# Optimization experiments

Hardware: AMD Instinct MI355X
Metric: run time of the kernel (lower is better)

## Reference

```python
import itertools
import jax, jax.numpy as jnp
import numpy as np

RES = 14
B = 64
DIM = 384
NH = 8
KD = 32
DV = 128  # attn_ratio * key_dim
SCALE = KD ** -0.5


def _bias_idxs(res):
    points = list(itertools.product(range(res), range(res)))
    offs, idxs = {}, []
    for p1 in points:
        for p2 in points:
            o = (abs(p1[0] - p2[0]), abs(p1[1] - p2[1]))
            if o not in offs:
                offs[o] = len(offs)
            idxs.append(offs[o])
    n = res * res
    return np.asarray(idxs, dtype=np.int32).reshape(n, n), len(offs)


def setup_inputs() -> dict:
    key = jax.random.key(0)
    ks = jax.random.split(key, 16)
    idxs, n_off = _bias_idxs(RES)  # n_off == 196 for res=14
    f = lambda k, shape, s=0.05: jax.random.normal(k, shape, dtype=jnp.float32) * s
    return {
        "x": jax.random.normal(ks[0], (B, DIM, RES, RES), dtype=jnp.float32),
        "qw": f(ks[1], (NH * KD, DIM)), "qb": f(ks[2], (NH * KD,)),
        "kw": f(ks[3], (NH * KD, DIM)), "kb": f(ks[4], (NH * KD,)),
        "vw": f(ks[5], (NH * DV, DIM)), "vb": f(ks[6], (NH * DV,)),
        "vlw": f(ks[7], (NH * DV, 1, 3, 3)), "vlb": f(ks[8], (NH * DV,)),
        "th1_w": f(ks[9], (NH, NH), 0.3), "th1_b": f(ks[10], (NH,)),
        "th2_w": f(ks[11], (NH, NH), 0.3), "th2_b": f(ks[12], (NH,)),
        "projw": f(ks[13], (DIM, NH * DV)), "projb": f(ks[14], (DIM,)),
        "bias_seg": f(ks[15], (NH, n_off), 0.5),
        "bias_idxs": jnp.asarray(idxs),
    }


def reference(x, qw, qb, kw, kb, vw, vb, vlw, vlb,
              th1_w, th1_b, th2_w, th2_b, projw, projb,
              bias_seg, bias_idxs):
    Bb, C, H, W = x.shape
    N = H * W
    xf = x.reshape(Bb, C, N)
    # 1x1 conv (+ folded BN) projections
    q = (jnp.einsum('oc,bcn->bon', qw, xf) + qb[:, None]).reshape(Bb, NH, KD, N).transpose(0, 1, 3, 2)  # [B,h,N,kd]
    k = (jnp.einsum('oc,bcn->bon', kw, xf) + kb[:, None]).reshape(Bb, NH, KD, N)                        # [B,h,kd,N]
    v4 = (jnp.einsum('oc,bcn->bon', vw, xf) + vb[:, None]).reshape(Bb, NH * DV, H, W)
    # depthwise 3x3 local branch (+ folded BN)
    v_local = jax.lax.conv_general_dilated(
        v4, vlw, window_strides=(1, 1), padding=[(1, 1), (1, 1)],
        dimension_numbers=('NCHW', 'OIHW', 'NCHW'), feature_group_count=NH * DV,
    ) + vlb[None, :, None, None]
    v = v4.reshape(Bb, NH, DV, N).transpose(0, 1, 3, 2)  # [B,h,N,dv]
    # attention scores + relative bias (bicubic interp 196->196 is identity)
    attn = jnp.einsum('bhnk,bhkm->bhnm', q, k) * SCALE
    bias = bias_seg[:, bias_idxs]  # [h,N,N]
    attn = attn + bias[None]
    # talking heads (1x1 conv over head dim) -> softmax -> talking heads
    attn = jnp.einsum('hg,bgnm->bhnm', th1_w, attn) + th1_b[None, :, None, None]
    attn = jax.nn.softmax(attn, axis=-1)
    attn = jnp.einsum('hg,bgnm->bhnm', th2_w, attn) + th2_b[None, :, None, None]
    o = jnp.einsum('bhnm,bhmd->bhnd', attn, v)           # [B,h,N,dv]
    o = o.transpose(0, 1, 3, 2).reshape(Bb, NH * DV, H, W) + v_local
    # proj: ReLU -> 1x1 conv (+ folded BN)
    o = jax.nn.relu(o)
    out = jnp.einsum('oc,bchw->bohw', projw, o) + projb[None, :, None, None]
    return out
```

## Files before the change

kernel.cpp:

```cpp
#include <hip/hip_runtime.h>
#include <hip/hip_bf16.h>


#define RES   14
#define NSP   196
#define NHD   8
#define KDIM  32
#define DVV   128
#define DIM   384
#define NQK   256
#define SCALE 0.17677669529663687f
#define SROW  224
#define NSTRIP 13

typedef __attribute__((ext_vector_type(8))) short bf16x8;
typedef __attribute__((ext_vector_type(4))) float f32x4;
typedef unsigned short u16;
typedef unsigned int u32;

__device__ __forceinline__ u16 f2b(float f) {
    union { __hip_bfloat16 b; u16 u; } c; c.b = __float2bfloat16(f); return c.u;
}
__device__ __forceinline__ float b2f(u16 u) {
    union { __hip_bfloat16 b; u16 u; } c; c.u = u; return __bfloat162float(c.b);
}

__device__ __forceinline__ void gld16(const void* g, void* l) {
    __builtin_amdgcn_global_load_lds(
        (__attribute__((address_space(1))) void*)(unsigned long long)(const char*)g,
        (__attribute__((address_space(3))) void*)l, 16, 0, 0);
}

__device__ __forceinline__ void gemm128_bk64(const char* Aseg, long rbA,
                                             const char* Bseg, long rbB, int kIters,
                                             u16* A_lds, u16* B_lds, f32x4 acc[4][4])
{
    const int tid  = threadIdx.x;
    const int wid  = tid >> 6;
    const int lane = tid & 63;
    const int lrow = lane >> 2;
    const int lcb  = (lane & 3) << 4;
    const int r0   = wid * 32;
    const int wm   = (wid & 1) * 64, wn = (wid >> 1) * 64;
    const int l15  = lane & 15, lq8 = (lane >> 4) * 8;

    #pragma unroll
    for (int i = 0; i < 4; ++i)
        #pragma unroll
        for (int j = 0; j < 4; ++j) acc[i][j] = (f32x4){0.f, 0.f, 0.f, 0.f};

    const char* ap0 = Aseg + (long)(r0 + lrow) * rbA + lcb;
    const char* ap1 = ap0 + 16 * rbA;
    const char* bp0 = Bseg + (long)(r0 + lrow) * rbB + lcb;
    const char* bp1 = bp0 + 16 * rbB;
    u16* la0 = A_lds + r0 * 32;
    u16* la1 = la0 + 512;
    u16* lb0 = B_lds + r0 * 32;
    u16* lb1 = lb0 + 512;

    for (int kk = 0; kk < kIters; ++kk) {
        gld16(ap0, la0);        gld16(ap1, la1);
        gld16(bp0, lb0);        gld16(bp1, lb1);
        gld16(ap0 + 64, la0 + 4096); gld16(ap1 + 64, la1 + 4096);
        gld16(bp0 + 64, lb0 + 4096); gld16(bp1 + 64, lb1 + 4096);
        ap0 += 128; ap1 += 128; bp0 += 128; bp1 += 128;
        __syncthreads();
        #pragma unroll
        for (int s = 0; s < 2; ++s) {
            bf16x8 af[4], bfr[4];
            #pragma unroll
            for (int i = 0; i < 4; ++i)
                af[i] = *(const bf16x8*)&A_lds[s * 4096 + (wm + i * 16 + l15) * 32 + lq8];
            #pragma unroll
            for (int j = 0; j < 4; ++j)
                bfr[j] = *(const bf16x8*)&B_lds[s * 4096 + (wn + j * 16 + l15) * 32 + lq8];
            #pragma unroll
            for (int i = 0; i < 4; ++i)
                #pragma unroll
                for (int j = 0; j < 4; ++j)
                    acc[i][j] = __builtin_amdgcn_mfma_f32_16x16x32_bf16(
                        af[i], bfr[j], acc[i][j], 0, 0, 0);
        }
        __syncthreads();
    }
}

__global__ __launch_bounds__(256) void k_prep(
    const float* __restrict__ qw, const float* __restrict__ kw,
    const float* __restrict__ vw, const float* __restrict__ pw,
    const float* __restrict__ th1w, const float* __restrict__ th1b,
    const float* __restrict__ bias_seg, const float* __restrict__ vlw,
    const float* __restrict__ x,
    u16* __restrict__ wqkv, u16* __restrict__ pwb, float* __restrict__ biasmix,
    u16* __restrict__ wpack, u16* __restrict__ xb)
{
    __shared__ float t[32][33];
    const int bid = blockIdx.x;
    if (bid < 3883) {
        int i = bid * 256 + threadIdx.x;
        if (i < 98304)       wqkv[i] = f2b(qw[i]);
        else if (i < 196608) wqkv[i] = f2b(kw[i - 98304]);
        else if (i < 589824) wqkv[i] = f2b(vw[i - 196608]);
        else if (i < 983040) pwb[i - 589824] = f2b(pw[i - 589824]);
        else if (i < 984608) {
            int i2 = i - 983040;
            int hh = i2 / NSP, off = i2 - hh * NSP;
            float a = th1b[hh];
            #pragma unroll
            for (int g = 0; g < 8; ++g) a += th1w[hh * 8 + g] * bias_seg[g * NSP + off];
            biasmix[i2] = a;
        } else if (i < 993824) {
            int i2 = i - 984608;
            int g = i2 / 72, r = i2 - g * 72;
            int tap = r >> 3, tt = r & 7;
            wpack[i2] = f2b(vlw[(g * 8 + tt) * 9 + tap]);
        }
    } else {
        const int L = bid - 3883;
        const int b = L / 84, r = L - b * 84;
        const int c0 = (r / 7) * 32, n0 = (r % 7) * 32;
        const int tx = threadIdx.x & 31, ty = threadIdx.x >> 5;
        #pragma unroll
        for (int l = 0; l < 4; ++l) {
            int c = c0 + ty + 8 * l, n = n0 + tx;
            t[ty + 8 * l][tx] = (n < NSP) ? x[((long)b * DIM + c) * NSP + n] : 0.f;
        }
        __syncthreads();
        #pragma unroll
        for (int l = 0; l < 4; ++l) {
            int n = n0 + ty + 8 * l, c = c0 + tx;
            if (n < NSP) xb[((long)b * NSP + n) * DIM + c] = f2b(t[tx][ty + 8 * l]);
        }
    }
}

__global__ __launch_bounds__(256) void k_qkv(
    const u16* __restrict__ xb, const u16* __restrict__ wqkv,
    const float* __restrict__ qb, const float* __restrict__ kb,
    const float* __restrict__ vb,
    u16* __restrict__ qt, u16* __restrict__ kb16, u16* __restrict__ vt)
{
    __shared__ u16 A_lds[8192], B_lds[8192];
    const int m0 = blockIdx.x * 128, oc0 = blockIdx.y * 128;
    f32x4 acc[4][4];
    gemm128_bk64((const char*)xb + (long)m0 * 768, 768,
                 (const char*)wqkv + (long)oc0 * 768, 768, 6, A_lds, B_lds, acc);

    const int tid = threadIdx.x, wid = tid >> 6, lane = tid & 63;
    const int wm = (wid & 1) * 64, wn = (wid >> 1) * 64;
    const int col = lane & 15, quad = lane >> 4;
    #pragma unroll
    for (int i = 0; i < 4; ++i) {
        #pragma unroll
        for (int j = 0; j < 4; ++j) {
            #pragma unroll
            for (int r = 0; r < 4; ++r) {
                int m  = m0 + wm + i * 16 + quad * 4 + r;
                int oc = oc0 + wn + j * 16 + col;
                int b = m / NSP, n = m - b * NSP;
                float v = acc[i][j][r];
                if (oc < 256) {
                    qt[(long)m * NQK + oc] = f2b(v + qb[oc]);
                } else if (oc < 512) {
                    int o = oc - 256;
                    kb16[(long)m * NQK + o] = f2b(v + kb[o]);
                } else {
                    int o = oc - 512, h = o >> 7, d = o & 127;
                    vt[(((long)b * NHD + h) * NSP + n) * DVV + d] = f2b(v + vb[o]);
                }
            }
        }
    }
}

__global__ __launch_bounds__(256) void k_vtT(
    const u16* __restrict__ vt, u16* __restrict__ vtT)
{
    __shared__ u16 t[32][33];
    const int bh = blockIdx.z, d0 = blockIdx.y * 32, n0 = blockIdx.x * 32;
    const int tx = threadIdx.x & 31, ty = threadIdx.x >> 5;
    #pragma unroll
    for (int l = 0; l < 4; ++l) {
        int n = n0 + ty + 8 * l, d = d0 + tx;
        t[ty + 8 * l][tx] = (n < NSP) ? vt[((long)bh * NSP + n) * DVV + d] : (u16)0;
    }
    __syncthreads();
    #pragma unroll
    for (int l = 0; l < 4; ++l) {
        int d = d0 + ty + 8 * l, m = n0 + tx;
        vtT[((long)bh * DVV + d) * 224 + m] = t[tx][ty + 8 * l];
    }
}

__global__ __launch_bounds__(256) void k_dwconv(
    const u16* __restrict__ vt, const u16* __restrict__ wpack,
    const float* __restrict__ vlb, u16* __restrict__ vlt)
{
    const int tid = threadIdx.x;
    const int dg = tid & 15;
    const int nl = tid >> 4;
    const int bh = blockIdx.y;
    const int n  = blockIdx.x * 16 + nl;
    if (n >= NSP) return;
    const int d0 = dg * 8;
    const int h  = bh & 7;
    const int y = n / RES, xx = n - y * RES;
    const long plane = (long)bh * NSP * DVV;
    float acc[8];
    #pragma unroll
    for (int t = 0; t < 8; ++t) acc[t] = vlb[h * DVV + d0 + t];
    const u16* wb = wpack + (h * 16 + dg) * 72;
    #pragma unroll
    for (int dy = -1; dy <= 1; ++dy) {
        int yy = y + dy;
        if (yy < 0 || yy >= RES) continue;
        #pragma unroll
        for (int dx = -1; dx <= 1; ++dx) {
            int xn = xx + dx;
            if (xn < 0 || xn >= RES) continue;
            int tap = (dy + 1) * 3 + dx + 1;
            bf16x8 v  = *(const bf16x8*)&vt[plane + (yy * RES + xn) * DVV + d0];
            bf16x8 wv = *(const bf16x8*)&wb[tap * 8];
            #pragma unroll
            for (int t = 0; t < 8; ++t)
                acc[t] += b2f((u16)wv[t]) * b2f((u16)v[t]);
        }
    }
    bf16x8 r;
    #pragma unroll
    for (int t = 0; t < 8; ++t) r[t] = (short)f2b(acc[t]);
    *(bf16x8*)&vlt[plane + (long)n * DVV + d0] = r;
}

__global__ __launch_bounds__(512, 2) void k_attn2(
    const u16* __restrict__ qt, const u16* __restrict__ kb16,
    const u16* __restrict__ vtT, const u16* __restrict__ vlt,
    const float* __restrict__ th1w, const float* __restrict__ th2w,
    const float* __restrict__ th2b, const float* __restrict__ biasmix,
    u16* __restrict__ ot)
{
    __shared__ u16 S[128 * SROW];
    __shared__ u16 bmS[8 * NSP];
    const int tid = threadIdx.x;
    const int L  = blockIdx.x;
    const int wq = L >> 3;
    const int b  = (L & 7) + ((wq / NSTRIP) << 3);
    const int n0 = (wq % NSTRIP) * 16;
    const int wid = tid >> 6, lane = tid & 63;
    const int l15 = lane & 15, lq8 = (lane >> 4) * 8;
    const int quad = lane >> 4, col = lane & 15;

    for (int i = tid; i < 8 * NSP; i += 512) bmS[i] = f2b(biasmix[i]);
    __syncthreads();

    {
        const long qrow = ((long)(b * NSP) + n0 + l15) * NQK;
        bf16x8 af[8];
        #pragma unroll
        for (int g = 0; g < 8; ++g)
            af[g] = *(const bf16x8*)&qt[qrow + g * 32 + lq8];
        #pragma unroll
        for (int jj = 0; jj < 2; ++jj) {
            const int j = wid + jj * 8;
            if (j >= 13) break;
            const long krow = ((long)(b * NSP) + j * 16 + l15) * NQK;
            f32x4 t[8];
            #pragma unroll
            for (int g = 0; g < 8; ++g) {
                bf16x8 bv = *(const bf16x8*)&kb16[krow + g * 32 + lq8];
                t[g] = __builtin_amdgcn_mfma_f32_16x16x32_bf16(
                    af[g], bv, (f32x4){0.f, 0.f, 0.f, 0.f}, 0, 0, 0);
            }
            const int m = j * 16 + col;
            const int ym = m / RES, xm = m - ym * RES;
            int offr[4];
            #pragma unroll
            for (int r = 0; r < 4; ++r) {
                int gn = n0 + quad * 4 + r;
                int yn = gn / RES, xn = gn - yn * RES;
                int off = abs(yn - ym) * RES + abs(xn - xm);
                offr[r] = (off > 195) ? 195 : off;
            }
            #pragma unroll
            for (int h = 0; h < 8; ++h) {
                float o[4];
                #pragma unroll
                for (int r = 0; r < 4; ++r) o[r] = b2f(bmS[h * NSP + offr[r]]);
                #pragma unroll
                for (int g = 0; g < 8; ++g) {
                    const float w = th1w[h * 8 + g] * SCALE;
                    #pragma unroll
                    for (int r = 0; r < 4; ++r) o[r] += w * t[g][r];
                }
                #pragma unroll
                for (int r = 0; r < 4; ++r)
                    S[(h * 16 + quad * 4 + r) * SROW + m] = f2b(o[r]);
            }
        }
    }
    __syncthreads();

    {
        const int c = lane & 15, rg = lane >> 4;
        #pragma unroll
        for (int it = 0; it < 4; ++it) {
            u16* row = &S[(wid * 16 + it * 4 + rg) * SROW];
            float v[13];
            #pragma unroll
            for (int k = 0; k < 12; ++k) v[k] = b2f(row[c + 16 * k]);
            v[12] = (c < 4) ? b2f(row[192 + c]) : -1e30f;
            float mx = v[0];
            #pragma unroll
            for (int k = 1; k < 13; ++k) mx = fmaxf(mx, v[k]);
            #pragma unroll
            for (int o = 1; o < 16; o <<= 1) mx = fmaxf(mx, __shfl_xor(mx, o));
            float sum = 0.f;
            #pragma unroll
            for (int k = 0; k < 13; ++k) { v[k] = __expf(v[k] - mx); sum += v[k]; }
            if (c >= 4) sum -= v[12];
            #pragma unroll
            for (int o = 1; o < 16; o <<= 1) sum += __shfl_xor(sum, o);
            float inv = 1.0f / sum;
            #pragma unroll
            for (int k = 0; k < 12; ++k) row[c + 16 * k] = f2b(v[k] * inv);
            if (c < 4) row[192 + c] = f2b(v[12] * inv);
        }
    }
    __syncthreads();

    {
        for (int p = tid; p < 16 * 112; p += 512) {
            const int nl = p / 112, kp = p - nl * 112;
            const int m0 = kp * 2;
            if (m0 >= NSP) {
                #pragma unroll
                for (int h = 0; h < 8; ++h)
                    *(u32*)&S[(h * 16 + nl) * SROW + m0] = 0u;
                continue;
            }
            float s0[8], s1[8];
            #pragma unroll
            for (int g = 0; g < 8; ++g) {
                u32 v = *(const u32*)&S[(g * 16 + nl) * SROW + m0];
                s0[g] = b2f((u16)(v & 0xffff));
                s1[g] = b2f((u16)(v >> 16));
            }
            #pragma unroll
            for (int h = 0; h < 8; ++h) {
                float o0 = th2b[h], o1 = th2b[h];
                #pragma unroll
                for (int g = 0; g < 8; ++g) {
                    const float w = th2w[h * 8 + g];
                    o0 += w * s0[g];
                    o1 += w * s1[g];
                }
                *(u32*)&S[(h * 16 + nl) * SROW + m0] =
                    (u32)f2b(o0) | ((u32)f2b(o1) << 16);
            }
        }
    }
    __syncthreads();

    {
        const int h = wid;
        const long vrow = (long)(b * NHD + h) * DVV;
        f32x4 acc[8];
        #pragma unroll
        for (int df = 0; df < 8; ++df) acc[df] = (f32x4){0.f, 0.f, 0.f, 0.f};
        for (int kc = 0; kc < 7; ++kc) {
            bf16x8 a0 = *(const bf16x8*)&S[(h * 16 + l15) * SROW + kc * 32 + lq8];
            #pragma unroll
            for (int df = 0; df < 8; ++df) {
                bf16x8 bv = *(const bf16x8*)&vtT[(vrow + df * 16 + l15) * 224 + kc * 32 + lq8];
                acc[df] = __builtin_amdgcn_mfma_f32_16x16x32_bf16(a0, bv, acc[df], 0, 0, 0);
            }
        }
        const long lbase = (long)(b * NHD + h) * NSP;
        #pragma unroll
        for (int df = 0; df < 8; ++df) {
            #pragma unroll
            for (int r = 0; r < 4; ++r) {
                int n = n0 + quad * 4 + r;
                int d = df * 16 + col;
                if (n < NSP) {
                    float v = acc[df][r] + b2f(vlt[(lbase + n) * DVV + d]);
                    v = fmaxf(v, 0.f);
                    ot[((long)(b * NSP + n)) * 1024 + h * DVV + d] = f2b(v);
                }
            }
        }
    }
}

__global__ __launch_bounds__(256) void k_proj(
    const u16* __restrict__ pwb, const u16* __restrict__ ot,
    const float* __restrict__ projb, float* __restrict__ outp)
{
    __shared__ u16 A_lds[8192];
    __shared__ u16 B_lds[4096];
    const int tid = threadIdx.x, wid = tid >> 6, lane = tid & 63;
    const int lrow = lane >> 2, lcb = (lane & 3) << 4;
    const int m0 = blockIdx.x * 64, oc0 = blockIdx.y * 128;
    const int wm = (wid & 1) * 64, wn = (wid >> 1) * 32;
    const int l15 = lane & 15, lq8 = (lane >> 4) * 8;

    const char* gp[6];
    u16* lp[6];
    #pragma unroll
    for (int t = 0; t < 6; ++t) {
        int s = wid * 6 + t;
        int sub = s / 12, s12 = s - sub * 12;
        if (s12 < 8) {
            gp[t] = (const char*)pwb + (long)(oc0 + s12 * 16 + lrow) * 2048 + lcb + sub * 64;
            lp[t] = A_lds + sub * 4096 + s12 * 512;
        } else {
            gp[t] = (const char*)ot + (long)(m0 + (s12 - 8) * 16 + lrow) * 2048 + lcb + sub * 64;
            lp[t] = B_lds + sub * 2048 + (s12 - 8) * 512;
        }
    }

    f32x4 acc[4][2];
    #pragma unroll
    for (int i = 0; i < 4; ++i)
        #pragma unroll
        for (int j = 0; j < 2; ++j) acc[i][j] = (f32x4){0.f, 0.f, 0.f, 0.f};

    for (int kk = 0; kk < 16; ++kk) {
        #pragma unroll
        for (int t = 0; t < 6; ++t) { gld16(gp[t], lp[t]); gp[t] += 128; }
        __syncthreads();
        #pragma unroll
        for (int s = 0; s < 2; ++s) {
            bf16x8 af[4], bfr[2];
            #pragma unroll
            for (int i = 0; i < 4; ++i)
                af[i] = *(const bf16x8*)&A_lds[s * 4096 + (wm + i * 16 + l15) * 32 + lq8];
            #pragma unroll
            for (int j = 0; j < 2; ++j)
                bfr[j] = *(const bf16x8*)&B_lds[s * 2048 + (wn + j * 16 + l15) * 32 + lq8];
            #pragma unroll
            for (int i = 0; i < 4; ++i)
                #pragma unroll
                for (int j = 0; j < 2; ++j)
                    acc[i][j] = __builtin_amdgcn_mfma_f32_16x16x32_bf16(
                        af[i], bfr[j], acc[i][j], 0, 0, 0);
        }
        __syncthreads();
    }

    const int col = lane & 15, quad = lane >> 4;
    #pragma unroll
    for (int i = 0; i < 4; ++i) {
        #pragma unroll
        for (int j = 0; j < 2; ++j) {
            #pragma unroll
            for (int r = 0; r < 4; ++r) {
                int oc = oc0 + wm + i * 16 + quad * 4 + r;
                int mg = m0 + wn + j * 16 + col;
                int b = mg / NSP, n = mg - b * NSP;
                outp[((long)b * DIM + oc) * NSP + n] = acc[i][j][r] + projb[oc];
            }
        }
    }
}

extern "C" void kernel_launch(void* const* d_in, const int* in_sizes, int n_in,
                              void* d_out, int out_size, void* d_ws, size_t ws_size,
                              hipStream_t stream) {
    const float* x        = (const float*)d_in[0];
    const float* qw       = (const float*)d_in[1];
    const float* qb       = (const float*)d_in[2];
    const float* kw       = (const float*)d_in[3];
    const float* kb       = (const float*)d_in[4];
    const float* vw       = (const float*)d_in[5];
    const float* vb       = (const float*)d_in[6];
    const float* vlw      = (const float*)d_in[7];
    const float* vlb      = (const float*)d_in[8];
    const float* th1w     = (const float*)d_in[9];
    const float* th1b     = (const float*)d_in[10];
    const float* th2w     = (const float*)d_in[11];
    const float* th2b     = (const float*)d_in[12];
    const float* projw    = (const float*)d_in[13];
    const float* projb    = (const float*)d_in[14];
    const float* bias_seg = (const float*)d_in[15];
    float* outp = (float*)d_out;

    char* w = (char*)d_ws;
    u16* xb      = (u16*)(w);
    u16* wqkv    = (u16*)(w + 9633792);
    u16* pwb     = (u16*)(w + 10813440);
    u16* wpack   = (u16*)(w + 11599872);
    float* bmix  = (float*)(w + 11618304);
    u16* qt      = (u16*)(w + 11624704);
    u16* kb16    = (u16*)(w + 18080000);
    u16* vt      = (u16*)(w + 24535296);
    u16* vtT     = (u16*)(w + 50225408);
    u16* ot      = (u16*)(w + 79585536);
    u16* vlt     = (u16*)(w + 105275648);

    k_prep<<<dim3(9259), 256, 0, stream>>>(qw, kw, vw, projw, th1w, th1b,
                                           bias_seg, vlw, x, wqkv, pwb, bmix,
                                           wpack, xb);
    k_qkv<<<dim3(98, 12), 256, 0, stream>>>(xb, wqkv, qb, kb, vb, qt, kb16, vt);
    k_vtT<<<dim3(7, 4, 512), 256, 0, stream>>>(vt, vtT);
    k_dwconv<<<dim3(13, 512), 256, 0, stream>>>(vt, wpack, vlb, vlt);
    k_attn2<<<dim3(NSTRIP * 64), 512, 0, stream>>>(qt, kb16, vtT, vlt, th1w, th2w,
                                                   th2b, bmix, ot);
    k_proj<<<dim3(196, 3), 256, 0, stream>>>(pwb, ot, projb, outp);
}
```

Baseline: 295.0 us.

## Merge V transpose and depthwise conv kernels, prefetch operands in attention, vectorize prep

Vectorizes the weight-conversion part of k_prep to float4 loads with 4-wide bf16 stores, which cuts its block count. Merges the V transpose and depthwise-conv kernels into one launch, and has the conv write its output transposed with row stride 208. Attention now issues the K loads for the second tile early and double-buffers the V operand loads across k-chunks. The epilogue reads the local branch as 4-wide vectors. The transposed conv store is a strided scalar write, which may be less coalesced than before.

```diff
diff --git a/kernel.cpp b/kernel.cpp
--- a/kernel.cpp
+++ b/kernel.cpp
@@ -11,10 +11,12 @@
 #define NQK   256
 #define SCALE 0.17677669529663687f
 #define SROW  224
+#define VROW  208
 #define NSTRIP 13
 
 typedef __attribute__((ext_vector_type(8))) short bf16x8;
 typedef __attribute__((ext_vector_type(4))) float f32x4;
+typedef __attribute__((ext_vector_type(4))) unsigned short u16x4;
 typedef unsigned short u16;
 typedef unsigned int u32;
 
@@ -96,27 +98,34 @@
 {
     __shared__ float t[32][33];
     const int bid = blockIdx.x;
-    if (bid < 3883) {
-        int i = bid * 256 + threadIdx.x;
-        if (i < 98304)       wqkv[i] = f2b(qw[i]);
-        else if (i < 196608) wqkv[i] = f2b(kw[i - 98304]);
-        else if (i < 589824) wqkv[i] = f2b(vw[i - 196608]);
-        else if (i < 983040) pwb[i - 589824] = f2b(pw[i - 589824]);
-        else if (i < 984608) {
-            int i2 = i - 983040;
+    if (bid < 960) {
+        const int i = (bid * 256 + threadIdx.x) * 4;
+        const float* src; u16* dst;
+        if (i < 98304)       { src = qw + i;            dst = wqkv + i; }
+        else if (i < 196608) { src = kw + (i - 98304);  dst = wqkv + i; }
+        else if (i < 589824) { src = vw + (i - 196608); dst = wqkv + i; }
+        else                 { src = pw + (i - 589824); dst = pwb + (i - 589824); }
+        float4 v = *(const float4*)src;
+        u16x4 o;
+        o[0] = f2b(v.x); o[1] = f2b(v.y); o[2] = f2b(v.z); o[3] = f2b(v.w);
+        *(u16x4*)dst = o;
+    } else if (bid == 960) {
+        for (int i2 = threadIdx.x; i2 < 8 * NSP; i2 += 256) {
             int hh = i2 / NSP, off = i2 - hh * NSP;
             float a = th1b[hh];
             #pragma unroll
             for (int g = 0; g < 8; ++g) a += th1w[hh * 8 + g] * bias_seg[g * NSP + off];
             biasmix[i2] = a;
-        } else if (i < 993824) {
-            int i2 = i - 984608;
+        }
+    } else if (bid < 997) {
+        int i2 = (bid - 961) * 256 + threadIdx.x;
+        if (i2 < 9216) {
             int g = i2 / 72, r = i2 - g * 72;
             int tap = r >> 3, tt = r & 7;
             wpack[i2] = f2b(vlw[(g * 8 + tt) * 9 + tap]);
         }
     } else {
-        const int L = bid - 3883;
+        const int L = bid - 997;
         const int b = L / 84, r = L - b * 84;
         const int c0 = (r / 7) * 32, n0 = (r % 7) * 32;
         const int tx = threadIdx.x & 31, ty = threadIdx.x >> 5;
@@ -173,68 +182,72 @@
     }
 }
 
-__global__ __launch_bounds__(256) void k_vtT(
-    const u16* __restrict__ vt, u16* __restrict__ vtT)
+__global__ __launch_bounds__(256) void k_vtdw(
+    const u16* __restrict__ vt, const u16* __restrict__ wpack,
+    const float* __restrict__ vlb,
+    u16* __restrict__ vtT, u16* __restrict__ vltT)
 {
     __shared__ u16 t[32][33];
-    const int bh = blockIdx.z, d0 = blockIdx.y * 32, n0 = blockIdx.x * 32;
-    const int tx = threadIdx.x & 31, ty = threadIdx.x >> 5;
-    #pragma unroll
-    for (int l = 0; l < 4; ++l) {
-        int n = n0 + ty + 8 * l, d = d0 + tx;
-        t[ty + 8 * l][tx] = (n < NSP) ? vt[((long)bh * NSP + n) * DVV + d] : (u16)0;
-    }
-    __syncthreads();
-    #pragma unroll
-    for (int l = 0; l < 4; ++l) {
-        int d = d0 + ty + 8 * l, m = n0 + tx;
-        vtT[((long)bh * DVV + d) * 224 + m] = t[tx][ty + 8 * l];
-    }
-}
-
-__global__ __launch_bounds__(256) void k_dwconv(
-    const u16* __restrict__ vt, const u16* __restrict__ wpack,
-    const float* __restrict__ vlb, u16* __restrict__ vlt)
-{
-    const int tid = threadIdx.x;
-    const int dg = tid & 15;
-    const int nl = tid >> 4;
-    const int bh = blockIdx.y;
-    const int n  = blockIdx.x * 16 + nl;
-    if (n >= NSP) return;
-    const int d0 = dg * 8;
-    const int h  = bh & 7;
-    const int y = n / RES, xx = n - y * RES;
-    const long plane = (long)bh * NSP * DVV;
-    float acc[8];
-    #pragma unroll
-    for (int t = 0; t < 8; ++t) acc[t] = vlb[h * DVV + d0 + t];
-    const u16* wb = wpack + (h * 16 + dg) * 72;
-    #pragma unroll
-    for (int dy = -1; dy <= 1; ++dy) {
-        int yy = y + dy;
-        if (yy < 0 || yy >= RES) continue;
-        #pragma unroll
-        for (int dx = -1; dx <= 1; ++dx) {
-            int xn = xx + dx;
-            if (xn < 0 || xn >= RES) continue;
-            int tap = (dy + 1) * 3 + dx + 1;
-            bf16x8 v  = *(const bf16x8*)&vt[plane + (yy * RES + xn) * DVV + d0];
-            bf16x8 wv = *(const bf16x8*)&wb[tap * 8];
-            #pragma unroll
-            for (int t = 0; t < 8; ++t)
-                acc[t] += b2f((u16)wv[t]) * b2f((u16)v[t]);
-        }
-    }
-    bf16x8 r;
-    #pragma unroll
-    for (int t = 0; t < 8; ++t) r[t] = (short)f2b(acc[t]);
-    *(bf16x8*)&vlt[plane + (long)n * DVV + d0] = r;
+    const int bid = blockIdx.x;
+    if (bid < 14336) {
+        const int n_i = bid % 7;
+        const int d_i = (bid / 7) & 3;
+        const int bh  = bid / 28;
+        const int d0 = d_i * 32, n0 = n_i * 32;
+        const int tx = threadIdx.x & 31, ty = threadIdx.x >> 5;
+        #pragma unroll
+        for (int l = 0; l < 4; ++l) {
+            int n = n0 + ty + 8 * l, d = d0 + tx;
+            t[ty + 8 * l][tx] = (n < NSP) ? vt[((long)bh * NSP + n) * DVV + d] : (u16)0;
+        }
+        __syncthreads();
+        #pragma unroll
+        for (int l = 0; l < 4; ++l) {
+            int d = d0 + ty + 8 * l, m = n0 + tx;
+            if (m < VROW) vtT[((long)bh * DVV + d) * VROW + m] = t[tx][ty + 8 * l];
+        }
+    } else {
+        const int b2 = bid - 14336;
+        const int nx = b2 % 13;
+        const int bh = b2 / 13;
+        const int tid = threadIdx.x;
+        const int dg = tid >> 4;
+        const int nl = tid & 15;
+        const int n  = nx * 16 + nl;
+        if (n >= NSP) return;
+        const int d0 = dg * 8;
+        const int h  = bh & 7;
+        const int y = n / RES, xx = n - y * RES;
+        const long plane = (long)bh * NSP * DVV;
+        float acc[8];
+        #pragma unroll
+        for (int k = 0; k < 8; ++k) acc[k] = vlb[h * DVV + d0 + k];
+        const u16* wb = wpack + (h * 16 + dg) * 72;
+        #pragma unroll
+        for (int dy = -1; dy <= 1; ++dy) {
+            int yy = y + dy;
+            if (yy < 0 || yy >= RES) continue;
+            #pragma unroll
+            for (int dx = -1; dx <= 1; ++dx) {
+                int xn = xx + dx;
+                if (xn < 0 || xn >= RES) continue;
+                int tap = (dy + 1) * 3 + dx + 1;
+                bf16x8 v  = *(const bf16x8*)&vt[plane + (yy * RES + xn) * DVV + d0];
+                bf16x8 wv = *(const bf16x8*)&wb[tap * 8];
+                #pragma unroll
+                for (int k = 0; k < 8; ++k)
+                    acc[k] += b2f((u16)wv[k]) * b2f((u16)v[k]);
+            }
+        }
+        #pragma unroll
+        for (int k = 0; k < 8; ++k)
+            vltT[((long)bh * DVV + d0 + k) * VROW + n] = f2b(acc[k]);
+    }
 }
 
 __global__ __launch_bounds__(512, 2) void k_attn2(
     const u16* __restrict__ qt, const u16* __restrict__ kb16,
-    const u16* __restrict__ vtT, const u16* __restrict__ vlt,
+    const u16* __restrict__ vtT, const u16* __restrict__ vltT,
     const float* __restrict__ th1w, const float* __restrict__ th2w,
     const float* __restrict__ th2b, const float* __restrict__ biasmix,
     u16* __restrict__ ot)
@@ -254,23 +267,7 @@
     __syncthreads();
 
     {
-        const long qrow = ((long)(b * NSP) + n0 + l15) * NQK;
-        bf16x8 af[8];
-        #pragma unroll
-        for (int g = 0; g < 8; ++g)
-            af[g] = *(const bf16x8*)&qt[qrow + g * 32 + lq8];
-        #pragma unroll
-        for (int jj = 0; jj < 2; ++jj) {
-            const int j = wid + jj * 8;
-            if (j >= 13) break;
-            const long krow = ((long)(b * NSP) + j * 16 + l15) * NQK;
-            f32x4 t[8];
-            #pragma unroll
-            for (int g = 0; g < 8; ++g) {
-                bf16x8 bv = *(const bf16x8*)&kb16[krow + g * 32 + lq8];
-                t[g] = __builtin_amdgcn_mfma_f32_16x16x32_bf16(
-                    af[g], bv, (f32x4){0.f, 0.f, 0.f, 0.f}, 0, 0, 0);
-            }
+        auto mix_store = [&](int j, f32x4 (&t)[8]) {
             const int m = j * 16 + col;
             const int ym = m / RES, xm = m - ym * RES;
             int offr[4];
@@ -296,6 +293,45 @@
                 for (int r = 0; r < 4; ++r)
                     S[(h * 16 + quad * 4 + r) * SROW + m] = f2b(o[r]);
             }
+        };
+
+        const long qrow = ((long)(b * NSP) + n0 + l15) * NQK;
+        bf16x8 af[8];
+        #pragma unroll
+        for (int g = 0; g < 8; ++g)
+            af[g] = *(const bf16x8*)&qt[qrow + g * 32 + lq8];
+
+        const int j0 = wid, j1 = wid + 8;
+        const bool has1 = (j1 < 13);
+        const long kr0 = ((long)(b * NSP) + j0 * 16 + l15) * NQK;
+
+        bf16x8 bv0[8];
+        #pragma unroll
+        for (int g = 0; g < 8; ++g)
+            bv0[g] = *(const bf16x8*)&kb16[kr0 + g * 32 + lq8];
+
+        f32x4 t[8];
+        #pragma unroll
+        for (int g = 0; g < 8; ++g)
+            t[g] = __builtin_amdgcn_mfma_f32_16x16x32_bf16(
+                af[g], bv0[g], (f32x4){0.f, 0.f, 0.f, 0.f}, 0, 0, 0);
+
+        bf16x8 bv1[8];
+        if (has1) {
+            const long kr1 = ((long)(b * NSP) + j1 * 16 + l15) * NQK;
+            #pragma unroll
+            for (int g = 0; g < 8; ++g)
+                bv1[g] = *(const bf16x8*)&kb16[kr1 + g * 32 + lq8];
+        }
+
+        mix_store(j0, t);
+
+        if (has1) {
+            #pragma unroll
+            for (int g = 0; g < 8; ++g)
+                t[g] = __builtin_amdgcn_mfma_f32_16x16x32_bf16(
+                    af[g], bv1[g], (f32x4){0.f, 0.f, 0.f, 0.f}, 0, 0, 0);
+            mix_store(j1, t);
         }
     }
     __syncthreads();
@@ -367,23 +403,36 @@
         f32x4 acc[8];
         #pragma unroll
         for (int df = 0; df < 8; ++df) acc[df] = (f32x4){0.f, 0.f, 0.f, 0.f};
+
+        bf16x8 bva[8], bvb[8];
+        #pragma unroll
+        for (int df = 0; df < 8; ++df)
+            bva[df] = *(const bf16x8*)&vtT[(vrow + df * 16 + l15) * VROW + lq8];
+
+        #pragma unroll
         for (int kc = 0; kc < 7; ++kc) {
+            const int kn = (kc < 6) ? kc + 1 : 6;
+            #pragma unroll
+            for (int df = 0; df < 8; ++df)
+                bvb[df] = *(const bf16x8*)&vtT[(vrow + df * 16 + l15) * VROW + kn * 32 + lq8];
             bf16x8 a0 = *(const bf16x8*)&S[(h * 16 + l15) * SROW + kc * 32 + lq8];
             #pragma unroll
-            for (int df = 0; df < 8; ++df) {
-                bf16x8 bv = *(const bf16x8*)&vtT[(vrow + df * 16 + l15) * 224 + kc * 32 + lq8];
-                acc[df] = __builtin_amdgcn_mfma_f32_16x16x32_bf16(a0, bv, acc[df], 0, 0, 0);
-            }
-        }
-        const long lbase = (long)(b * NHD + h) * NSP;
+            for (int df = 0; df < 8; ++df)
+                acc[df] = __builtin_amdgcn_mfma_f32_16x16x32_bf16(a0, bva[df], acc[df], 0, 0, 0);
+            #pragma unroll
+            for (int df = 0; df < 8; ++df) bva[df] = bvb[df];
+        }
+
+        const long vl = (long)(b * NHD + h) * DVV;
         #pragma unroll
         for (int df = 0; df < 8; ++df) {
+            const int d = df * 16 + col;
+            u16x4 lv = *(const u16x4*)&vltT[(vl + d) * VROW + n0 + quad * 4];
             #pragma unroll
             for (int r = 0; r < 4; ++r) {
                 int n = n0 + quad * 4 + r;
-                int d = df * 16 + col;
                 if (n < NSP) {
-                    float v = acc[df][r] + b2f(vlt[(lbase + n) * DVV + d]);
+                    float v = acc[df][r] + b2f((u16)lv[r]);
                     v = fmaxf(v, 0.f);
                     ot[((long)(b * NSP + n)) * 1024 + h * DVV + d] = f2b(v);
                 }
@@ -495,16 +544,15 @@
     u16* kb16    = (u16*)(w + 18080000);
     u16* vt      = (u16*)(w + 24535296);
     u16* vtT     = (u16*)(w + 50225408);
-    u16* ot      = (u16*)(w + 79585536);
-    u16* vlt     = (u16*)(w + 105275648);
-
-    k_prep<<<dim3(9259), 256, 0, stream>>>(qw, kw, vw, projw, th1w, th1b,
+    u16* ot      = (u16*)(w + 77488384);
+    u16* vltT    = (u16*)(w + 103178496);
+
+    k_prep<<<dim3(6373), 256, 0, stream>>>(qw, kw, vw, projw, th1w, th1b,
                                            bias_seg, vlw, x, wqkv, pwb, bmix,
                                            wpack, xb);
     k_qkv<<<dim3(98, 12), 256, 0, stream>>>(xb, wqkv, qb, kb, vb, qt, kb16, vt);
-    k_vtT<<<dim3(7, 4, 512), 256, 0, stream>>>(vt, vtT);
-    k_dwconv<<<dim3(13, 512), 256, 0, stream>>>(vt, wpack, vlb, vlt);
-    k_attn2<<<dim3(NSTRIP * 64), 512, 0, stream>>>(qt, kb16, vtT, vlt, th1w, th2w,
+    k_vtdw<<<dim3(20992), 256, 0, stream>>>(vt, wpack, vlb, vtT, vltT);
+    k_attn2<<<dim3(NSTRIP * 64), 512, 0, stream>>>(qt, kb16, vtT, vltT, th1w, th2w,
                                                    th2b, bmix, ot);
     k_proj<<<dim3(196, 3), 256, 0, stream>>>(pwb, ot, projb, outp);
 }
```

New measurement: 345.3 us. 17.1% more time.
